# Performance work log

Measured on AMD Instinct MI355X. Metric: run time of the kernel, lower is better.

Reference implementation:

```python
import jax, jax.numpy as jnp
import numpy as np
import math

B, S, D, H = 4, 2048, 512, 8
HD = D // H  # head dim = 64

def setup_inputs() -> dict:
    key = jax.random.key(0)
    ks = jax.random.split(key, 12)
    inp = {
        'queries': jax.random.normal(ks[0], (B, S, D), jnp.float32),
        'keys': jax.random.normal(ks[1], (B, S, D), jnp.float32),
        'values': jax.random.normal(ks[2], (B, S, D), jnp.float32),
        'valid_lens': jax.random.randint(ks[3], (B,), 0, 2048, jnp.int32),
        'Wq': jax.random.normal(ks[4], (D, D), jnp.float32) / math.sqrt(D),
        'bq': jnp.zeros((D,), jnp.float32),
        'Wk': jax.random.normal(ks[5], (D, D), jnp.float32) / math.sqrt(D),
        'bk': jnp.zeros((D,), jnp.float32),
        'Wv': jax.random.normal(ks[6], (D, D), jnp.float32) / math.sqrt(D),
        'bv': jnp.zeros((D,), jnp.float32),
        'Wo': jax.random.normal(ks[7], (D, D), jnp.float32) / math.sqrt(D),
        'bo': jnp.zeros((D,), jnp.float32),
    }
    return inp

def reference(queries, keys, values, valid_lens, Wq, bq, Wk, bk, Wv, bv, Wo, bo):
    # project and split heads: [B,S,D] -> [B,H,S,HD]
    def split_heads(x):
        return x.reshape(B, S, H, HD).transpose(0, 2, 1, 3)
    q = split_heads(queries @ Wq + bq)
    k = split_heads(keys @ Wk + bk)
    v = split_heads(values @ Wv + bv)
    # scores [B,H,Sq,Sk]
    scores = jnp.einsum('bhqd,bhkd->bhqk', q, k) / math.sqrt(HD)
    # masked softmax: mask key positions >= valid_len with -1e6 (d2l semantics)
    mask = jnp.arange(S)[None, None, None, :] < valid_lens[:, None, None, None]
    scores = jnp.where(mask, scores, -1e6)
    attn = jax.nn.softmax(scores, axis=-1)
    out = jnp.einsum('bhqk,bhkd->bhqd', attn, v)  # [B,H,S,HD]
    out = out.transpose(0, 2, 1, 3).reshape(B, S, D)
    return out @ Wo + bo
```

## Files before the change

### kernel.cpp

```cpp
#include <hip/hip_runtime.h>
#include <hip/hip_bf16.h>

typedef _Float16 half8 __attribute__((ext_vector_type(8)));
typedef float floatx4 __attribute__((ext_vector_type(4)));

#define LOG2E 1.44269504088896340736f

__device__ __forceinline__ half8 cvt8(const float* p) {
    floatx4 a = *(const floatx4*)p;
    floatx4 b = *(const floatx4*)(p + 4);
    half8 h;
    h[0] = (_Float16)a[0]; h[1] = (_Float16)a[1]; h[2] = (_Float16)a[2]; h[3] = (_Float16)a[3];
    h[4] = (_Float16)b[0]; h[5] = (_Float16)b[1]; h[6] = (_Float16)b[2]; h[7] = (_Float16)b[3];
    return h;
}

__global__ __launch_bounds__(256) void transpose_w_kernel(
        const float* __restrict__ Wq, const float* __restrict__ Wk,
        const float* __restrict__ Wv, const float* __restrict__ Wo,
        _Float16* __restrict__ out) {
    const float* W = (blockIdx.z == 0) ? Wq : (blockIdx.z == 1) ? Wk : (blockIdx.z == 2) ? Wv : Wo;
    _Float16* o = out + (size_t)blockIdx.z * 512 * 512;
    __shared__ __align__(16) _Float16 t[64][72];
    int r0 = blockIdx.x * 64, c0 = blockIdx.y * 64;
    int tid = threadIdx.x;
    for (int i = 0; i < 2; i++) {
        int f = i * 256 + tid;
        int row = f >> 3, seg = f & 7;
        *(half8*)&t[row][seg * 8] = cvt8(W + (size_t)(r0 + row) * 512 + c0 + seg * 8);
    }
    __syncthreads();
    for (int i = 0; i < 2; i++) {
        int f = i * 256 + tid;
        int crow = f >> 3, seg = f & 7;
        half8 hv;
        for (int j = 0; j < 8; j++) hv[j] = t[seg * 8 + j][crow];
        *(half8*)(o + (size_t)(c0 + crow) * 512 + r0 + seg * 8) = hv;
    }
}

__global__ __launch_bounds__(256) void gemm_qkv_kernel(
        const float* __restrict__ Xq, const float* __restrict__ Xk, const float* __restrict__ Xv,
        const _Float16* __restrict__ WTall,
        const float* __restrict__ bq, const float* __restrict__ bk, const float* __restrict__ bv,
        _Float16* __restrict__ qo, _Float16* __restrict__ ko2, _Float16* __restrict__ vo) {
    int z = blockIdx.z;
    const float* X = (z == 0) ? Xq : (z == 1) ? Xk : Xv;
    const _Float16* BT = WTall + (size_t)z * 512 * 512;
    const float* bias = (z == 0) ? bq : (z == 1) ? bk : bv;
    _Float16* out = (z == 0) ? qo : (z == 1) ? ko2 : vo;

    __shared__ __align__(16) _Float16 Asm[128][72];
    __shared__ __align__(16) _Float16 Bsm[128][72];

    int tid = threadIdx.x;
    int wave = tid >> 6, lane = tid & 63;
    int lrow = lane & 15, quad = lane >> 4;
    int m0 = (wave >> 1) * 64, n0 = (wave & 1) * 64;
    int mBase = blockIdx.x * 128, nBase = blockIdx.y * 128;

    const floatx4 fz = {0.f, 0.f, 0.f, 0.f};
    floatx4 acc[4][4];
    for (int i = 0; i < 4; i++) for (int j = 0; j < 4; j++) acc[i][j] = fz;

    for (int kb = 0; kb < 512; kb += 64) {
        for (int i = 0; i < 4; i++) {
            int f = i * 256 + tid;
            int row = f >> 3, seg = f & 7;
            *(half8*)&Asm[row][seg * 8] = cvt8(X + (size_t)(mBase + row) * 512 + kb + seg * 8);
            *(half8*)&Bsm[row][seg * 8] = *(const half8*)(BT + (size_t)(nBase + row) * 512 + kb + seg * 8);
        }
        __syncthreads();
        for (int kc = 0; kc < 2; kc++) {
            int ko_ = kc * 32 + quad * 8;
            half8 a[4], b[4];
            for (int mt = 0; mt < 4; mt++) a[mt] = *(const half8*)&Asm[m0 + mt * 16 + lrow][ko_];
            for (int nt = 0; nt < 4; nt++) b[nt] = *(const half8*)&Bsm[n0 + nt * 16 + lrow][ko_];
            for (int mt = 0; mt < 4; mt++)
                for (int nt = 0; nt < 4; nt++)
                    acc[mt][nt] = __builtin_amdgcn_mfma_f32_16x16x32_f16(a[mt], b[nt], acc[mt][nt], 0, 0, 0);
        }
        __syncthreads();
    }

    for (int nt = 0; nt < 4; nt++) {
        int gc = nBase + n0 + nt * 16 + lrow;
        float bb = bias[gc];
        int h = gc >> 6, hd = gc & 63;
        for (int mt = 0; mt < 4; mt++) {
            for (int r = 0; r < 4; r++) {
                int gr = mBase + m0 + mt * 16 + quad * 4 + r;
                int b_ = gr >> 11, s = gr & 2047;
                out[(((size_t)b_ * 8 + h) * 2048 + s) * 64 + hd] = (_Float16)(acc[mt][nt][r] + bb);
            }
        }
    }
}

__global__ __launch_bounds__(256) void transpose_v_kernel(
        const _Float16* __restrict__ v, _Float16* __restrict__ vt) {
    int bh = blockIdx.z;
    int s0 = blockIdx.x * 64;
    __shared__ __align__(16) _Float16 t[64][72];
    int tid = threadIdx.x;
    for (int i = 0; i < 2; i++) {
        int f = i * 256 + tid;
        int row = f >> 3, seg = f & 7;
        *(half8*)&t[row][seg * 8] = *(const half8*)(v + ((size_t)bh * 2048 + s0 + row) * 64 + seg * 8);
    }
    __syncthreads();
    for (int i = 0; i < 2; i++) {
        int f = i * 256 + tid;
        int crow = f >> 3, seg = f & 7;
        half8 hv;
        for (int j = 0; j < 8; j++) hv[j] = t[seg * 8 + j][crow];
        *(half8*)(vt + ((size_t)bh * 64 + crow) * 2048 + s0 + seg * 8) = hv;
    }
}

__global__ __launch_bounds__(256) void attn_kernel(
        const _Float16* __restrict__ qws, const _Float16* __restrict__ kws, const _Float16* __restrict__ vtws,
        const int* __restrict__ vlens, _Float16* __restrict__ aout) {
    int bh = blockIdx.y;
    int b = bh >> 3, h = bh & 7;
    int q0 = blockIdx.x * 128;
    int L = vlens[b];
    bool uni = (L == 0);
    int nkt = uni ? 32 : ((L + 63) >> 6);
    int tid = threadIdx.x;
    int wave = tid >> 6, lane = tid & 63;
    int lrow = lane & 15, quad = lane >> 4;

    __shared__ __align__(16) _Float16 ksm[64][72];
    __shared__ __align__(16) _Float16 vtsm[80][72];
    __shared__ __align__(16) _Float16 psm[4][2][16][72];

    for (int i = tid; i < 16 * 36; i += 256) {
        int r = i / 36, c = i % 36;
        ((float*)&vtsm[64 + r][0])[c] = 0.0f;
    }
    if (tid < 64) vtsm[64][tid] = (_Float16)1.0f;

    const _Float16* qbase = qws + ((size_t)bh * 2048 + q0) * 64;
    const _Float16* kbase = kws + (size_t)bh * 2048 * 64;
    const _Float16* vtbase = vtws + (size_t)bh * 64 * 2048;

    half8 aq[2][2];
    for (int mt = 0; mt < 2; mt++)
        for (int kc = 0; kc < 2; kc++)
            aq[mt][kc] = *(const half8*)(qbase + (wave * 32 + mt * 16 + lrow) * 64 + kc * 32 + quad * 8);

    const floatx4 fz = {0.f, 0.f, 0.f, 0.f};
    floatx4 oacc[2][5];
    for (int mt = 0; mt < 2; mt++) for (int nt = 0; nt < 5; nt++) oacc[mt][nt] = fz;

    const float cexp = 0.125f * LOG2E;

    for (int kt = 0; kt < nkt; kt++) {
        const _Float16* ktile = kbase + (size_t)kt * 64 * 64;
        const _Float16* vttile = vtbase + kt * 64;
        for (int i = 0; i < 2; i++) {
            int f = i * 256 + tid;
            int row = f >> 3, seg = f & 7;
            *(half8*)&ksm[row][seg * 8] = *(const half8*)(ktile + f * 8);
            *(half8*)&vtsm[row][seg * 8] = *(const half8*)(vttile + (size_t)row * 2048 + seg * 8);
        }
        __syncthreads();

        floatx4 sacc[2][4];
        for (int mt = 0; mt < 2; mt++) for (int nt = 0; nt < 4; nt++) sacc[mt][nt] = fz;
        for (int kc = 0; kc < 2; kc++) {
            int ko_ = kc * 32 + quad * 8;
            half8 bk[4];
            for (int nt = 0; nt < 4; nt++) bk[nt] = *(const half8*)&ksm[nt * 16 + lrow][ko_];
            for (int mt = 0; mt < 2; mt++)
                for (int nt = 0; nt < 4; nt++)
                    sacc[mt][nt] = __builtin_amdgcn_mfma_f32_16x16x32_f16(aq[mt][kc], bk[nt], sacc[mt][nt], 0, 0, 0);
        }

        for (int nt = 0; nt < 4; nt++) {
            int col = kt * 64 + nt * 16 + lrow;
            bool valid = col < L;
            for (int mt = 0; mt < 2; mt++) {
                for (int r = 0; r < 4; r++) {
                    float p = uni ? 1.0f : (valid ? exp2f(sacc[mt][nt][r] * cexp) : 0.0f);
                    psm[wave][mt][quad * 4 + r][nt * 16 + lrow] = (_Float16)p;
                }
            }
        }

        for (int kc = 0; kc < 2; kc++) {
            int ko_ = kc * 32 + quad * 8;
            half8 ap[2];
            for (int mt = 0; mt < 2; mt++) ap[mt] = *(const half8*)&psm[wave][mt][lrow][ko_];
            for (int nt = 0; nt < 5; nt++) {
                half8 bv = *(const half8*)&vtsm[nt * 16 + lrow][ko_];
                for (int mt = 0; mt < 2; mt++)
                    oacc[mt][nt] = __builtin_amdgcn_mfma_f32_16x16x32_f16(ap[mt], bv, oacc[mt][nt], 0, 0, 0);
            }
        }
        __syncthreads();
    }

    float inv[2][4];
    for (int mt = 0; mt < 2; mt++)
        for (int r = 0; r < 4; r++)
            inv[mt][r] = 1.0f / __shfl(oacc[mt][4][r], (lane & 48), 64);

    for (int mt = 0; mt < 2; mt++) {
        for (int nt = 0; nt < 4; nt++) {
            for (int r = 0; r < 4; r++) {
                int s = q0 + wave * 32 + mt * 16 + quad * 4 + r;
                aout[((size_t)b * 2048 + s) * 512 + h * 64 + nt * 16 + lrow] =
                    (_Float16)(oacc[mt][nt][r] * inv[mt][r]);
            }
        }
    }
}

__global__ __launch_bounds__(256) void gemm_out_kernel(
        const _Float16* __restrict__ A, const _Float16* __restrict__ BT,
        const float* __restrict__ bias, float* __restrict__ out) {
    __shared__ __align__(16) _Float16 Asm[128][72];
    __shared__ __align__(16) _Float16 Bsm[128][72];

    int tid = threadIdx.x;
    int wave = tid >> 6, lane = tid & 63;
    int lrow = lane & 15, quad = lane >> 4;
    int m0 = (wave >> 1) * 64, n0 = (wave & 1) * 64;
    int mBase = blockIdx.x * 128, nBase = blockIdx.y * 128;

    const floatx4 fz = {0.f, 0.f, 0.f, 0.f};
    floatx4 acc[4][4];
    for (int i = 0; i < 4; i++) for (int j = 0; j < 4; j++) acc[i][j] = fz;

    for (int kb = 0; kb < 512; kb += 64) {
        for (int i = 0; i < 4; i++) {
            int f = i * 256 + tid;
            int row = f >> 3, seg = f & 7;
            *(half8*)&Asm[row][seg * 8] = *(const half8*)(A + (size_t)(mBase + row) * 512 + kb + seg * 8);
            *(half8*)&Bsm[row][seg * 8] = *(const half8*)(BT + (size_t)(nBase + row) * 512 + kb + seg * 8);
        }
        __syncthreads();
        for (int kc = 0; kc < 2; kc++) {
            int ko_ = kc * 32 + quad * 8;
            half8 a[4], b[4];
            for (int mt = 0; mt < 4; mt++) a[mt] = *(const half8*)&Asm[m0 + mt * 16 + lrow][ko_];
            for (int nt = 0; nt < 4; nt++) b[nt] = *(const half8*)&Bsm[n0 + nt * 16 + lrow][ko_];
            for (int mt = 0; mt < 4; mt++)
                for (int nt = 0; nt < 4; nt++)
                    acc[mt][nt] = __builtin_amdgcn_mfma_f32_16x16x32_f16(a[mt], b[nt], acc[mt][nt], 0, 0, 0);
        }
        __syncthreads();
    }

    for (int nt = 0; nt < 4; nt++) {
        int gc = nBase + n0 + nt * 16 + lrow;
        float bb = bias[gc];
        for (int mt = 0; mt < 4; mt++) {
            for (int r = 0; r < 4; r++) {
                int gr = mBase + m0 + mt * 16 + quad * 4 + r;
                out[(size_t)gr * 512 + gc] = acc[mt][nt][r] + bb;
            }
        }
    }
}

extern "C" void kernel_launch(void* const* d_in, const int* in_sizes, int n_in,
                              void* d_out, int out_size, void* d_ws, size_t ws_size,
                              hipStream_t stream) {
    const float* Q  = (const float*)d_in[0];
    const float* K  = (const float*)d_in[1];
    const float* V  = (const float*)d_in[2];
    const int*   VL = (const int*)d_in[3];
    const float* Wq = (const float*)d_in[4];
    const float* bq = (const float*)d_in[5];
    const float* Wk = (const float*)d_in[6];
    const float* bk = (const float*)d_in[7];
    const float* Wv = (const float*)d_in[8];
    const float* bv = (const float*)d_in[9];
    const float* Wo = (const float*)d_in[10];
    const float* bo = (const float*)d_in[11];

    char* ws = (char*)d_ws;
    _Float16* WT   = (_Float16*)ws;
    _Float16* qws  = (_Float16*)(ws + (size_t)(2)  * 1024 * 1024);
    _Float16* kws  = (_Float16*)(ws + (size_t)(10) * 1024 * 1024);
    _Float16* vws  = (_Float16*)(ws + (size_t)(18) * 1024 * 1024);
    _Float16* vtws = (_Float16*)(ws + (size_t)(26) * 1024 * 1024);
    _Float16* aout = vws;

    transpose_w_kernel<<<dim3(8, 8, 4), 256, 0, stream>>>(Wq, Wk, Wv, Wo, WT);
    gemm_qkv_kernel<<<dim3(64, 4, 3), 256, 0, stream>>>(Q, K, V, WT, bq, bk, bv, qws, kws, vws);
    transpose_v_kernel<<<dim3(32, 1, 32), 256, 0, stream>>>(vws, vtws);
    attn_kernel<<<dim3(16, 32, 1), 256, 0, stream>>>(qws, kws, vtws, VL, aout);
    gemm_out_kernel<<<dim3(64, 4, 1), 256, 0, stream>>>(aout, WT + (size_t)3 * 512 * 512, bo, (float*)d_out);
}
```

Before: 226.9 us.

## Fuse V transpose into QKV GEMM and keep attention probabilities in registers

The QKV projection now writes V directly in transposed [b,h,d,s] layout with 4-wide stores, which removes the separate transpose_v kernel. The attention kernel computes S^T = K·Q^T so that the MFMA output layout feeds straight into a 16x16x16 MFMA as the A operand. This eliminates the shared-memory round trip for the probability tile. Each block now handles 64 queries instead of 128 (1024 blocks), and the block index is swizzled to spread batches with different valid lengths across the grid. The trade-offs are more K/V tile reloads per query, the smaller-K MFMA instruction for P·V, and strided transposed stores from the GEMM.

```diff
diff --git a/kernel.cpp b/kernel.cpp
--- a/kernel.cpp
+++ b/kernel.cpp
@@ -2,6 +2,7 @@
 #include <hip/hip_bf16.h>
 
 typedef _Float16 half8 __attribute__((ext_vector_type(8)));
+typedef _Float16 half4 __attribute__((ext_vector_type(4)));
 typedef float floatx4 __attribute__((ext_vector_type(4)));
 
 #define LOG2E 1.44269504088896340736f
@@ -43,12 +44,11 @@
         const float* __restrict__ Xq, const float* __restrict__ Xk, const float* __restrict__ Xv,
         const _Float16* __restrict__ WTall,
         const float* __restrict__ bq, const float* __restrict__ bk, const float* __restrict__ bv,
-        _Float16* __restrict__ qo, _Float16* __restrict__ ko2, _Float16* __restrict__ vo) {
+        _Float16* __restrict__ qo, _Float16* __restrict__ ko2, _Float16* __restrict__ vto) {
     int z = blockIdx.z;
     const float* X = (z == 0) ? Xq : (z == 1) ? Xk : Xv;
     const _Float16* BT = WTall + (size_t)z * 512 * 512;
     const float* bias = (z == 0) ? bq : (z == 1) ? bk : bv;
-    _Float16* out = (z == 0) ? qo : (z == 1) ? ko2 : vo;
 
     __shared__ __align__(16) _Float16 Asm[128][72];
     __shared__ __align__(16) _Float16 Bsm[128][72];
@@ -83,47 +83,44 @@
         __syncthreads();
     }
 
-    for (int nt = 0; nt < 4; nt++) {
-        int gc = nBase + n0 + nt * 16 + lrow;
-        float bb = bias[gc];
-        int h = gc >> 6, hd = gc & 63;
-        for (int mt = 0; mt < 4; mt++) {
-            for (int r = 0; r < 4; r++) {
-                int gr = mBase + m0 + mt * 16 + quad * 4 + r;
+    if (z == 2) {
+        for (int nt = 0; nt < 4; nt++) {
+            int gc = nBase + n0 + nt * 16 + lrow;
+            float bb = bias[gc];
+            int h = gc >> 6, hd = gc & 63;
+            for (int mt = 0; mt < 4; mt++) {
+                int gr = mBase + m0 + mt * 16 + quad * 4;
                 int b_ = gr >> 11, s = gr & 2047;
-                out[(((size_t)b_ * 8 + h) * 2048 + s) * 64 + hd] = (_Float16)(acc[mt][nt][r] + bb);
-            }
-        }
-    }
-}
-
-__global__ __launch_bounds__(256) void transpose_v_kernel(
-        const _Float16* __restrict__ v, _Float16* __restrict__ vt) {
-    int bh = blockIdx.z;
-    int s0 = blockIdx.x * 64;
-    __shared__ __align__(16) _Float16 t[64][72];
-    int tid = threadIdx.x;
-    for (int i = 0; i < 2; i++) {
-        int f = i * 256 + tid;
-        int row = f >> 3, seg = f & 7;
-        *(half8*)&t[row][seg * 8] = *(const half8*)(v + ((size_t)bh * 2048 + s0 + row) * 64 + seg * 8);
-    }
-    __syncthreads();
-    for (int i = 0; i < 2; i++) {
-        int f = i * 256 + tid;
-        int crow = f >> 3, seg = f & 7;
-        half8 hv;
-        for (int j = 0; j < 8; j++) hv[j] = t[seg * 8 + j][crow];
-        *(half8*)(vt + ((size_t)bh * 64 + crow) * 2048 + s0 + seg * 8) = hv;
+                half4 hv;
+                for (int r = 0; r < 4; r++) hv[r] = (_Float16)(acc[mt][nt][r] + bb);
+                *(half4*)(vto + (((size_t)(b_ * 8 + h) * 64 + hd) * 2048 + s)) = hv;
+            }
+        }
+    } else {
+        _Float16* out = (z == 0) ? qo : ko2;
+        for (int nt = 0; nt < 4; nt++) {
+            int gc = nBase + n0 + nt * 16 + lrow;
+            float bb = bias[gc];
+            int h = gc >> 6, hd = gc & 63;
+            for (int mt = 0; mt < 4; mt++) {
+                for (int r = 0; r < 4; r++) {
+                    int gr = mBase + m0 + mt * 16 + quad * 4 + r;
+                    int b_ = gr >> 11, s = gr & 2047;
+                    out[(((size_t)b_ * 8 + h) * 2048 + s) * 64 + hd] = (_Float16)(acc[mt][nt][r] + bb);
+                }
+            }
+        }
     }
 }
 
 __global__ __launch_bounds__(256) void attn_kernel(
         const _Float16* __restrict__ qws, const _Float16* __restrict__ kws, const _Float16* __restrict__ vtws,
         const int* __restrict__ vlens, _Float16* __restrict__ aout) {
-    int bh = blockIdx.y;
-    int b = bh >> 3, h = bh & 7;
-    int q0 = blockIdx.x * 128;
+    int idx = blockIdx.x;
+    int b = ((idx & 3) + (idx >> 8)) & 3;
+    int h = (idx >> 2) & 7;
+    int q0 = ((idx >> 5) & 31) * 64;
+    int bh = b * 8 + h;
     int L = vlens[b];
     bool uni = (L == 0);
     int nkt = uni ? 32 : ((L + 63) >> 6);
@@ -133,11 +130,10 @@
 
     __shared__ __align__(16) _Float16 ksm[64][72];
     __shared__ __align__(16) _Float16 vtsm[80][72];
-    __shared__ __align__(16) _Float16 psm[4][2][16][72];
-
-    for (int i = tid; i < 16 * 36; i += 256) {
+
+    for (int i = tid; i < 15 * 36; i += 256) {
         int r = i / 36, c = i % 36;
-        ((float*)&vtsm[64 + r][0])[c] = 0.0f;
+        ((float*)&vtsm[65 + r][0])[c] = 0.0f;
     }
     if (tid < 64) vtsm[64][tid] = (_Float16)1.0f;
 
@@ -145,15 +141,13 @@
     const _Float16* kbase = kws + (size_t)bh * 2048 * 64;
     const _Float16* vtbase = vtws + (size_t)bh * 64 * 2048;
 
-    half8 aq[2][2];
-    for (int mt = 0; mt < 2; mt++)
-        for (int kc = 0; kc < 2; kc++)
-            aq[mt][kc] = *(const half8*)(qbase + (wave * 32 + mt * 16 + lrow) * 64 + kc * 32 + quad * 8);
+    half8 qf[2];
+    for (int kc = 0; kc < 2; kc++)
+        qf[kc] = *(const half8*)(qbase + (wave * 16 + lrow) * 64 + kc * 32 + quad * 8);
 
     const floatx4 fz = {0.f, 0.f, 0.f, 0.f};
-    floatx4 oacc[2][5];
-    for (int mt = 0; mt < 2; mt++) for (int nt = 0; nt < 5; nt++) oacc[mt][nt] = fz;
-
+    floatx4 oacc[5];
+    for (int nt = 0; nt < 5; nt++) oacc[nt] = fz;
     const float cexp = 0.125f * LOG2E;
 
     for (int kt = 0; kt < nkt; kt++) {
@@ -167,53 +161,45 @@
         }
         __syncthreads();
 
-        floatx4 sacc[2][4];
-        for (int mt = 0; mt < 2; mt++) for (int nt = 0; nt < 4; nt++) sacc[mt][nt] = fz;
+        floatx4 sacc[4];
+        for (int km = 0; km < 4; km++) sacc[km] = fz;
         for (int kc = 0; kc < 2; kc++) {
             int ko_ = kc * 32 + quad * 8;
-            half8 bk[4];
-            for (int nt = 0; nt < 4; nt++) bk[nt] = *(const half8*)&ksm[nt * 16 + lrow][ko_];
-            for (int mt = 0; mt < 2; mt++)
-                for (int nt = 0; nt < 4; nt++)
-                    sacc[mt][nt] = __builtin_amdgcn_mfma_f32_16x16x32_f16(aq[mt][kc], bk[nt], sacc[mt][nt], 0, 0, 0);
-        }
-
-        for (int nt = 0; nt < 4; nt++) {
-            int col = kt * 64 + nt * 16 + lrow;
-            bool valid = col < L;
-            for (int mt = 0; mt < 2; mt++) {
-                for (int r = 0; r < 4; r++) {
-                    float p = uni ? 1.0f : (valid ? exp2f(sacc[mt][nt][r] * cexp) : 0.0f);
-                    psm[wave][mt][quad * 4 + r][nt * 16 + lrow] = (_Float16)p;
-                }
-            }
-        }
-
-        for (int kc = 0; kc < 2; kc++) {
-            int ko_ = kc * 32 + quad * 8;
-            half8 ap[2];
-            for (int mt = 0; mt < 2; mt++) ap[mt] = *(const half8*)&psm[wave][mt][lrow][ko_];
+            for (int km = 0; km < 4; km++) {
+                half8 kf = *(const half8*)&ksm[km * 16 + lrow][ko_];
+                sacc[km] = __builtin_amdgcn_mfma_f32_16x16x32_f16(kf, qf[kc], sacc[km], 0, 0, 0);
+            }
+        }
+
+        half4 pf[4];
+        int kb0 = kt * 64 + quad * 4;
+        for (int km = 0; km < 4; km++) {
+            int kb = kb0 + km * 16;
+            for (int r = 0; r < 4; r++) {
+                float p = uni ? 1.0f : ((kb + r < L) ? exp2f(sacc[km][r] * cexp) : 0.0f);
+                pf[km][r] = (_Float16)p;
+            }
+        }
+
+        for (int km = 0; km < 4; km++) {
+            int kk = km * 16 + quad * 4;
             for (int nt = 0; nt < 5; nt++) {
-                half8 bv = *(const half8*)&vtsm[nt * 16 + lrow][ko_];
-                for (int mt = 0; mt < 2; mt++)
-                    oacc[mt][nt] = __builtin_amdgcn_mfma_f32_16x16x32_f16(ap[mt], bv, oacc[mt][nt], 0, 0, 0);
-            }
-        }
-        __syncthreads();
-    }
-
-    float inv[2][4];
-    for (int mt = 0; mt < 2; mt++)
-        for (int r = 0; r < 4; r++)
-            inv[mt][r] = 1.0f / __shfl(oacc[mt][4][r], (lane & 48), 64);
-
-    for (int mt = 0; mt < 2; mt++) {
-        for (int nt = 0; nt < 4; nt++) {
-            for (int r = 0; r < 4; r++) {
-                int s = q0 + wave * 32 + mt * 16 + quad * 4 + r;
-                aout[((size_t)b * 2048 + s) * 512 + h * 64 + nt * 16 + lrow] =
-                    (_Float16)(oacc[mt][nt][r] * inv[mt][r]);
-            }
+                half4 bvf = *(const half4*)&vtsm[nt * 16 + lrow][kk];
+                oacc[nt] = __builtin_amdgcn_mfma_f32_16x16x16f16(pf[km], bvf, oacc[nt], 0, 0, 0);
+            }
+        }
+        __syncthreads();
+    }
+
+    float inv[4];
+    for (int r = 0; r < 4; r++)
+        inv[r] = 1.0f / __shfl(oacc[4][r], quad << 4, 64);
+
+    for (int nt = 0; nt < 4; nt++) {
+        for (int r = 0; r < 4; r++) {
+            int s = q0 + wave * 16 + quad * 4 + r;
+            aout[((size_t)b * 2048 + s) * 512 + h * 64 + nt * 16 + lrow] =
+                (_Float16)(oacc[nt][r] * inv[r]);
         }
     }
 }
@@ -286,13 +272,11 @@
     _Float16* WT   = (_Float16*)ws;
     _Float16* qws  = (_Float16*)(ws + (size_t)(2)  * 1024 * 1024);
     _Float16* kws  = (_Float16*)(ws + (size_t)(10) * 1024 * 1024);
-    _Float16* vws  = (_Float16*)(ws + (size_t)(18) * 1024 * 1024);
+    _Float16* aout = (_Float16*)(ws + (size_t)(18) * 1024 * 1024);
     _Float16* vtws = (_Float16*)(ws + (size_t)(26) * 1024 * 1024);
-    _Float16* aout = vws;
 
     transpose_w_kernel<<<dim3(8, 8, 4), 256, 0, stream>>>(Wq, Wk, Wv, Wo, WT);
-    gemm_qkv_kernel<<<dim3(64, 4, 3), 256, 0, stream>>>(Q, K, V, WT, bq, bk, bv, qws, kws, vws);
-    transpose_v_kernel<<<dim3(32, 1, 32), 256, 0, stream>>>(vws, vtws);
-    attn_kernel<<<dim3(16, 32, 1), 256, 0, stream>>>(qws, kws, vtws, VL, aout);
+    gemm_qkv_kernel<<<dim3(64, 4, 3), 256, 0, stream>>>(Q, K, V, WT, bq, bk, bv, qws, kws, vtws);
+    attn_kernel<<<dim3(1024, 1, 1), 256, 0, stream>>>(qws, kws, vtws, VL, aout);
     gemm_out_kernel<<<dim3(64, 4, 1), 256, 0, stream>>>(aout, WT + (size_t)3 * 512 * 512, bo, (float*)d_out);
 }
```

New measurement: 206.9 us. 8.8% less time.
